# Kernel optimization log

Hardware: AMD Instinct MI355X
Metric: run time of the kernel (lower is better)

## Reference

```python
import jax, jax.numpy as jnp
import numpy as np

CONSTRAINT_WEIGHT = 0.5
FOCAL_GAMMA = 2.0
EPS = 1e-8

B, G, C = 65536, 9, 9
BLK = 3  # int(sqrt(G))


def setup_inputs() -> dict:
    key = jax.random.key(0)
    k1, k2, k3 = jax.random.split(key, 3)
    logits = jax.random.normal(k1, (B, G, G, C), dtype=jnp.float32)
    targets = jax.random.randint(k2, (B, G, G), 0, 10, dtype=jnp.int64)
    puzzles = jax.random.randint(k3, (B, G, G), 0, 10, dtype=jnp.int64)
    return {"logits": logits, "targets": targets, "puzzles": puzzles}


def _sudoku_loss(logits, targets, puzzles):
    b, g, _, c = logits.shape
    mask = (puzzles == 0).astype(logits.dtype)            # [B,G,G]
    tgt = jnp.clip(targets - 1, 0, c - 1)                 # [B,G,G]

    log_probs = jax.nn.log_softmax(logits, axis=-1)       # [B,G,G,C]
    probs = jnp.exp(log_probs)

    # --- focal CE over masked (empty) cells ---
    lp_t = jnp.take_along_axis(log_probs, tgt[..., None], axis=-1)[..., 0]  # [B,G,G]
    pt = jnp.exp(lp_t)
    ce = -lp_t
    focal = (1.0 - pt) ** FOCAL_GAMMA * ce
    msum = mask.sum()
    ce_loss = (focal * mask).sum() / (msum + EPS)

    # --- constraint loss ---
    masked_probs = probs * mask[..., None]                # [B,G,G,C]
    row_sums = masked_probs.sum(axis=2)                   # [B,G,C]
    row_loss = jnp.mean((row_sums - 1.0) ** 2)
    col_sums = masked_probs.sum(axis=1)                   # [B,G,C]
    col_loss = jnp.mean((col_sums - 1.0) ** 2)
    # boxes: [B, br, r, bc, c_in, C] -> sum over the 3x3 cells of each box
    box = masked_probs.reshape(b, BLK, BLK, BLK, BLK, c)
    box_sums = box.transpose(0, 1, 3, 2, 4, 5).reshape(b, BLK * BLK, BLK * BLK, c).sum(axis=2)
    box_loss = jnp.mean((box_sums - 1.0) ** 2)

    entropy = -(probs * log_probs).sum(axis=-1)           # [B,G,G]
    entropy_loss = 0.1 * ((entropy * mask).sum() / (msum + EPS))

    top2, _ = jax.lax.top_k(probs, 2)                     # [B,G,G,2]
    gap = top2[..., 0] - top2[..., 1]
    uniqueness_loss = 0.1 * jnp.mean(jax.nn.relu(1.0 - gap))

    constraint_loss = (row_loss + col_loss + box_loss + entropy_loss + uniqueness_loss) * 0.2
    return ce_loss + CONSTRAINT_WEIGHT * constraint_loss


def reference(logits, targets, puzzles):
    return _sudoku_loss(logits, targets, puzzles)
```

## Files before the change

kernel.cpp:

```cpp
#include <hip/hip_runtime.h>

#define THREADS 256
#define PB 8
#define CELLS_PB (PB * 81)
#define TOTW (CELLS_PB * 9)
#define NF4 (TOTW / 4)
#define SLANES 243
#define WLANES 162

typedef float f4 __attribute__((ext_vector_type(4)));
typedef __fp16 h2 __attribute__((ext_vector_type(2)));
typedef unsigned int u32;
typedef int i4 __attribute__((ext_vector_type(4)));

static __device__ __forceinline__ u32 pkrtz(float a, float b) {
  h2 v = __builtin_amdgcn_cvt_pkrtz(a, b);
  return __builtin_bit_cast(u32, v);
}

__global__ __launch_bounds__(THREADS) void sudoku_main(
    const float* __restrict__ logits,
    const int*   __restrict__ targets,
    const int*   __restrict__ puzzles,
    float* __restrict__ partial,
    int B, int ngrid)
{
  __shared__ float buf[TOTW];
  __shared__ float sred[4][5];

  const int tid = threadIdx.x;
  const int g   = blockIdx.x;
  const long totalCells = (long)B * 81;
  const long lim4 = totalCells * 9 / 4;

  float a_focal=0.f, a_ent=0.f, a_msk=0.f, a_uniq=0.f, a_sq=0.f;

  if (tid < SLANES) {
    const f4* src = (const f4*)logits;
    const long b4 = (long)g * NF4;
    f4* dst = (f4*)buf;
#pragma unroll
    for (int r = 0; r < 6; ++r) {
      long idx = b4 + r * SLANES + tid;
      if (idx < lim4) dst[r * SLANES + tid] = src[idx];
    }
  }

  const long cell0 = (long)g * CELLS_PB + 4 * tid;
  const bool vA = (tid < WLANES) && (cell0 < totalCells);
  i4 tg4{}, pz4{};
  if (vA) {
    tg4 = *(const i4*)(targets + cell0);
    pz4 = *(const i4*)(puzzles + cell0);
  }
  __syncthreads();

  if (vA) {
    f4 s[9];
#pragma unroll
    for (int q = 0; q < 9; ++q) s[q] = ((const f4*)buf)[tid * 9 + q];

#pragma unroll
    for (int k = 0; k < 4; ++k) {
      float l[9];
#pragma unroll
      for (int i = 0; i < 9; ++i) { const int w = 9 * k + i; l[i] = s[w >> 2][w & 3]; }
      int tg = tg4[k] - 1; tg = tg < 0 ? 0 : (tg > 8 ? 8 : tg);

      float t1 = l[0], t2 = -3.0e38f;
#pragma unroll
      for (int i = 1; i < 9; ++i) {
        float hi = fmaxf(t1, l[i]);
        float lo = fminf(t1, l[i]);
        t1 = hi; t2 = fmaxf(t2, lo);
      }
      float e[9], ssum = 0.f, lsum = 0.f, ltg = l[0];
#pragma unroll
      for (int i = 0; i < 9; ++i) {
        float x  = l[i] - t1;
        float ei = __expf(x);
        e[i] = ei; ssum += ei;
        lsum = fmaf(ei, x, lsum);
        if (i > 0) ltg = (tg == i) ? l[i] : ltg;
      }
      float inv_s = __builtin_amdgcn_rcpf(ssum);
      float logs  = __logf(ssum);
      float lpt   = (ltg - t1) - logs;
      float pt    = __expf(lpt);
      float om    = 1.f - pt;
      float focal = om * om * (-lpt);
      float ent   = logs - lsum * inv_s;
      float gap   = (1.f - __expf(t2 - t1)) * inv_s;
      float uq    = fmaxf(0.f, 1.f - gap);
      float mk    = (pz4[k] == 0) ? 1.f : 0.f;
      a_focal += focal * mk;
      a_ent   += ent * mk;
      a_msk   += mk;
      a_uniq  += uq;
      float pm = inv_s * mk;

      u32* pw = (u32*)buf + (size_t)(4 * tid + k) * 9;
      pw[0] = pkrtz(e[0] * pm, e[1] * pm);
      pw[1] = pkrtz(e[2] * pm, e[3] * pm);
      pw[2] = pkrtz(e[4] * pm, e[5] * pm);
      pw[3] = pkrtz(e[6] * pm, e[7] * pm);
      pw[4] = pkrtz(e[8] * pm, 0.f);
    }
  }
  __syncthreads();

  const int wv = tid >> 6, lane = tid & 63;
  if (lane < 10) {
    const int pz = wv * 2 + lane / 5;
    const int pr = lane % 5;
    if ((long)g * PB + pz < (long)B) {
      const u32* cb = (const u32*)buf;
      h2 hz; hz[0] = (__fp16)0.f; hz[1] = (__fp16)0.f;
      h2 rs[9], cs[9], bs[9];
#pragma unroll
      for (int u = 0; u < 9; ++u) { rs[u] = hz; cs[u] = hz; bs[u] = hz; }
      const int base = pz * 729 + pr;
#pragma unroll
      for (int j = 0; j < 81; ++j) {
        h2 v = __builtin_bit_cast(h2, cb[base + 9 * j]);
        rs[j / 9]                      += v;
        cs[j % 9]                      += v;
        bs[(j / 27) * 3 + (j % 9) / 3] += v;
      }
      const float hiw = (pr == 4) ? 0.f : 1.f;
      float sq = 0.f;
#pragma unroll
      for (int u = 0; u < 9; ++u) {
        float x;
        x = (float)rs[u][0] - 1.f; sq = fmaf(x, x, sq);
        x = (float)cs[u][0] - 1.f; sq = fmaf(x, x, sq);
        x = (float)bs[u][0] - 1.f; sq = fmaf(x, x, sq);
        x = (float)rs[u][1] - 1.f; sq = fmaf(hiw * x, x, sq);
        x = (float)cs[u][1] - 1.f; sq = fmaf(hiw * x, x, sq);
        x = (float)bs[u][1] - 1.f; sq = fmaf(hiw * x, x, sq);
      }
      a_sq += sq;
    }
  }

#pragma unroll
  for (int off = 32; off > 0; off >>= 1) {
    a_focal += __shfl_down(a_focal, off);
    a_ent   += __shfl_down(a_ent,   off);
    a_msk   += __shfl_down(a_msk,   off);
    a_uniq  += __shfl_down(a_uniq,  off);
    a_sq    += __shfl_down(a_sq,    off);
  }
  if (lane == 0) {
    sred[wv][0] = a_focal; sred[wv][1] = a_ent; sred[wv][2] = a_msk;
    sred[wv][3] = a_uniq;  sred[wv][4] = a_sq;
  }
  __syncthreads();
  if (tid < 5) {
    float v = sred[0][tid] + sred[1][tid] + sred[2][tid] + sred[3][tid];
    partial[(size_t)tid * ngrid + g] = v;
  }
}

__global__ __launch_bounds__(1024) void sudoku_finalize(
    const float* __restrict__ partial, float* __restrict__ out,
    int ngrid, float invBG)
{
  __shared__ float sb[16][5];
  const int tid = threadIdx.x;
  float s[5] = {0.f, 0.f, 0.f, 0.f, 0.f};
  for (int b = tid; b < ngrid; b += 1024) {
#pragma unroll
    for (int u = 0; u < 5; ++u) s[u] += partial[(size_t)u * ngrid + b];
  }
#pragma unroll
  for (int off = 32; off > 0; off >>= 1)
#pragma unroll
    for (int u = 0; u < 5; ++u) s[u] += __shfl_down(s[u], off);
  const int wv = tid >> 6, lane = tid & 63;
  if (lane == 0) {
#pragma unroll
    for (int u = 0; u < 5; ++u) sb[wv][u] = s[u];
  }
  __syncthreads();
  if (tid == 0) {
    float focal = 0.f, ent = 0.f, msum = 0.f, uniq = 0.f, sq = 0.f;
#pragma unroll
    for (int w = 0; w < 16; ++w) {
      focal += sb[w][0]; ent += sb[w][1]; msum += sb[w][2];
      uniq  += sb[w][3]; sq  += sb[w][4];
    }
    float inv_m = 1.f / (msum + 1e-8f);
    float ce    = focal * inv_m;
    float entl  = 0.1f * ent * inv_m;
    float uql   = 0.1f * uniq * invBG;
    float rcb   = sq * invBG;
    float constraint = (rcb + entl + uql) * 0.2f;
    out[0] = ce + 0.5f * constraint;
  }
}

extern "C" void kernel_launch(void* const* d_in, const int* in_sizes, int n_in,
                              void* d_out, int out_size, void* d_ws, size_t ws_size,
                              hipStream_t stream)
{
  (void)n_in; (void)out_size; (void)ws_size;
  const float* logits  = (const float*)d_in[0];
  const int*   targets = (const int*)d_in[1];
  const int*   puzzles = (const int*)d_in[2];
  float* out = (float*)d_out;
  float* partial = (float*)d_ws;

  const int B = in_sizes[0] / 729;
  const long totalCells = (long)B * 81;
  const int ngrid = (int)((totalCells + CELLS_PB - 1) / CELLS_PB);

  sudoku_main<<<ngrid, THREADS, 0, stream>>>(logits, targets, puzzles, partial, B, ngrid);

  const float invBG = 1.f / ((float)B * 81.f);
  sudoku_finalize<<<1, 1024, 0, stream>>>(partial, out, ngrid, invBG);
}
```

Before: 67.72 us.

## Use 512-thread blocks of 12 puzzles, two cells per thread, exp2-based softmax

Blocks grow to 512 threads covering 12 puzzles, so each worker thread processes two cells instead of four and all threads take part in the staging load. Softmax, log and focal terms move to base-2 hardware exp2/log with LN2 rescaling, and packed probabilities are written back with vectorized shared-memory stores. The box/row/column reduction is remapped to 8 lanes per wave across 8 waves. This raises per-block parallelism and cuts per-thread register pressure, but uses more LDS per block (about 35 KB), which may limit how many blocks fit on a CU.

```diff
diff --git a/kernel.cpp b/kernel.cpp
--- a/kernel.cpp
+++ b/kernel.cpp
@@ -1,24 +1,28 @@
 #include <hip/hip_runtime.h>
 
-#define THREADS 256
-#define PB 8
+#define THREADS 512
+#define PB 12
 #define CELLS_PB (PB * 81)
 #define TOTW (CELLS_PB * 9)
 #define NF4 (TOTW / 4)
-#define SLANES 243
-#define WLANES 162
+#define WLANES 486
 
 typedef float f4 __attribute__((ext_vector_type(4)));
+typedef float f2 __attribute__((ext_vector_type(2)));
 typedef __fp16 h2 __attribute__((ext_vector_type(2)));
 typedef unsigned int u32;
-typedef int i4 __attribute__((ext_vector_type(4)));
+typedef u32 u2 __attribute__((ext_vector_type(2)));
+typedef int i2 __attribute__((ext_vector_type(2)));
+
+#define LOG2E 1.44269504f
+#define LN2   0.69314718f
 
 static __device__ __forceinline__ u32 pkrtz(float a, float b) {
   h2 v = __builtin_amdgcn_cvt_pkrtz(a, b);
   return __builtin_bit_cast(u32, v);
 }
 
-__global__ __launch_bounds__(THREADS) void sudoku_main(
+__global__ __launch_bounds__(THREADS, 8) void sudoku_main(
     const float* __restrict__ logits,
     const int*   __restrict__ targets,
     const int*   __restrict__ puzzles,
@@ -26,7 +30,7 @@
     int B, int ngrid)
 {
   __shared__ float buf[TOTW];
-  __shared__ float sred[4][5];
+  __shared__ float sred[8][5];
 
   const int tid = threadIdx.x;
   const int g   = blockIdx.x;
@@ -35,37 +39,44 @@
 
   float a_focal=0.f, a_ent=0.f, a_msk=0.f, a_uniq=0.f, a_sq=0.f;
 
-  if (tid < SLANES) {
+  {
     const f4* src = (const f4*)logits;
     const long b4 = (long)g * NF4;
     f4* dst = (f4*)buf;
 #pragma unroll
-    for (int r = 0; r < 6; ++r) {
-      long idx = b4 + r * SLANES + tid;
-      if (idx < lim4) dst[r * SLANES + tid] = src[idx];
-    }
-  }
-
-  const long cell0 = (long)g * CELLS_PB + 4 * tid;
+    for (int r = 0; r < 4; ++r) {
+      long idx = b4 + r * THREADS + tid;
+      if (idx < lim4) dst[r * THREADS + tid] = src[idx];
+    }
+    if (tid < NF4 - 4 * THREADS) {
+      long idx = b4 + 4 * THREADS + tid;
+      if (idx < lim4) dst[4 * THREADS + tid] = src[idx];
+    }
+  }
+
+  const long cell0 = (long)g * CELLS_PB + 2 * tid;
   const bool vA = (tid < WLANES) && (cell0 < totalCells);
-  i4 tg4{}, pz4{};
+  i2 tg2{}, pz2{};
   if (vA) {
-    tg4 = *(const i4*)(targets + cell0);
-    pz4 = *(const i4*)(puzzles + cell0);
+    tg2 = *(const i2*)(targets + cell0);
+    pz2 = *(const i2*)(puzzles + cell0);
   }
   __syncthreads();
 
   if (vA) {
-    f4 s[9];
-#pragma unroll
-    for (int q = 0; q < 9; ++q) s[q] = ((const f4*)buf)[tid * 9 + q];
-
-#pragma unroll
-    for (int k = 0; k < 4; ++k) {
+    f2 v[9];
+    const f2* xp = (const f2*)(buf + 18 * tid);
+#pragma unroll
+    for (int q = 0; q < 9; ++q) v[q] = xp[q];
+
+    u32 q5[2][5];
+#pragma unroll
+    for (int k = 0; k < 2; ++k) {
       float l[9];
 #pragma unroll
-      for (int i = 0; i < 9; ++i) { const int w = 9 * k + i; l[i] = s[w >> 2][w & 3]; }
-      int tg = tg4[k] - 1; tg = tg < 0 ? 0 : (tg > 8 ? 8 : tg);
+      for (int i = 0; i < 9; ++i) { const int w = 9 * k + i; l[i] = v[w >> 1][w & 1]; }
+      int tg = ((k == 0) ? tg2[0] : tg2[1]) - 1; tg = tg < 0 ? 0 : (tg > 8 ? 8 : tg);
+      const int pz = (k == 0) ? pz2[0] : pz2[1];
 
       float t1 = l[0], t2 = -3.0e38f;
 #pragma unroll
@@ -74,72 +85,81 @@
         float lo = fminf(t1, l[i]);
         t1 = hi; t2 = fmaxf(t2, lo);
       }
-      float e[9], ssum = 0.f, lsum = 0.f, ltg = l[0];
+      const float t1b = t1 * LOG2E;
+      float e[9], ssum = 0.f, lsum2 = 0.f, x2tg = 0.f;
 #pragma unroll
       for (int i = 0; i < 9; ++i) {
-        float x  = l[i] - t1;
-        float ei = __expf(x);
+        float x2 = fmaf(l[i], LOG2E, -t1b);
+        float ei = __builtin_amdgcn_exp2f(x2);
         e[i] = ei; ssum += ei;
-        lsum = fmaf(ei, x, lsum);
-        if (i > 0) ltg = (tg == i) ? l[i] : ltg;
+        lsum2 = fmaf(ei, x2, lsum2);
+        x2tg = (tg == i) ? x2 : x2tg;
       }
       float inv_s = __builtin_amdgcn_rcpf(ssum);
-      float logs  = __logf(ssum);
-      float lpt   = (ltg - t1) - logs;
-      float pt    = __expf(lpt);
+      float logs2 = __builtin_amdgcn_logf(ssum);
+      float lptb  = x2tg - logs2;
+      float pt    = __builtin_amdgcn_exp2f(lptb);
       float om    = 1.f - pt;
-      float focal = om * om * (-lpt);
-      float ent   = logs - lsum * inv_s;
-      float gap   = (1.f - __expf(t2 - t1)) * inv_s;
+      float focal = om * om * (-lptb * LN2);
+      float ent   = (logs2 - lsum2 * inv_s) * LN2;
+      float g2    = __builtin_amdgcn_exp2f(fmaf(t2, LOG2E, -t1b));
+      float gap   = (1.f - g2) * inv_s;
       float uq    = fmaxf(0.f, 1.f - gap);
-      float mk    = (pz4[k] == 0) ? 1.f : 0.f;
+      float mk    = (pz == 0) ? 1.f : 0.f;
       a_focal += focal * mk;
       a_ent   += ent * mk;
       a_msk   += mk;
       a_uniq  += uq;
       float pm = inv_s * mk;
-
-      u32* pw = (u32*)buf + (size_t)(4 * tid + k) * 9;
-      pw[0] = pkrtz(e[0] * pm, e[1] * pm);
-      pw[1] = pkrtz(e[2] * pm, e[3] * pm);
-      pw[2] = pkrtz(e[4] * pm, e[5] * pm);
-      pw[3] = pkrtz(e[6] * pm, e[7] * pm);
-      pw[4] = pkrtz(e[8] * pm, 0.f);
-    }
+      q5[k][0] = pkrtz(e[0]*pm, e[1]*pm);
+      q5[k][1] = pkrtz(e[2]*pm, e[3]*pm);
+      q5[k][2] = pkrtz(e[4]*pm, e[5]*pm);
+      q5[k][3] = pkrtz(e[6]*pm, e[7]*pm);
+      q5[k][4] = pkrtz(e[8]*pm, 0.f);
+    }
+    u32* wp = (u32*)(buf + 18 * tid);
+    { u2 a; a[0]=q5[0][0]; a[1]=q5[0][1]; *(u2*)(wp + 0) = a; }
+    { u2 a; a[0]=q5[0][2]; a[1]=q5[0][3]; *(u2*)(wp + 2) = a; }
+    wp[4] = q5[0][4];
+    wp[9] = q5[1][0];
+    { u2 a; a[0]=q5[1][1]; a[1]=q5[1][2]; *(u2*)(wp + 10) = a; }
+    { u2 a; a[0]=q5[1][3]; a[1]=q5[1][4]; *(u2*)(wp + 12) = a; }
   }
   __syncthreads();
 
   const int wv = tid >> 6, lane = tid & 63;
-  if (lane < 10) {
-    const int pz = wv * 2 + lane / 5;
-    const int pr = lane % 5;
-    if ((long)g * PB + pz < (long)B) {
-      const u32* cb = (const u32*)buf;
-      h2 hz; hz[0] = (__fp16)0.f; hz[1] = (__fp16)0.f;
-      h2 rs[9], cs[9], bs[9];
-#pragma unroll
-      for (int u = 0; u < 9; ++u) { rs[u] = hz; cs[u] = hz; bs[u] = hz; }
-      const int base = pz * 729 + pr;
-#pragma unroll
-      for (int j = 0; j < 81; ++j) {
-        h2 v = __builtin_bit_cast(h2, cb[base + 9 * j]);
-        rs[j / 9]                      += v;
-        cs[j % 9]                      += v;
-        bs[(j / 27) * 3 + (j % 9) / 3] += v;
+  if (lane < 8) {
+    const int q = wv * 8 + lane;
+    if (q < PB * 5) {
+      const int pz = q / 5, pr = q % 5;
+      if ((long)g * PB + pz < (long)B) {
+        const u32* cb = (const u32*)buf;
+        h2 hz; hz[0] = (__fp16)0.f; hz[1] = (__fp16)0.f;
+        h2 rs[9], cs[9], bs[9];
+#pragma unroll
+        for (int u = 0; u < 9; ++u) { rs[u] = hz; cs[u] = hz; bs[u] = hz; }
+        const int base = pz * 729 + pr;
+#pragma unroll
+        for (int j = 0; j < 81; ++j) {
+          h2 pv = __builtin_bit_cast(h2, cb[base + 9 * j]);
+          rs[j / 9]                      += pv;
+          cs[j % 9]                      += pv;
+          bs[(j / 27) * 3 + (j % 9) / 3] += pv;
+        }
+        const float hiw = (pr == 4) ? 0.f : 1.f;
+        float sq = 0.f;
+#pragma unroll
+        for (int u = 0; u < 9; ++u) {
+          float x;
+          x = (float)rs[u][0] - 1.f; sq = fmaf(x, x, sq);
+          x = (float)cs[u][0] - 1.f; sq = fmaf(x, x, sq);
+          x = (float)bs[u][0] - 1.f; sq = fmaf(x, x, sq);
+          x = (float)rs[u][1] - 1.f; sq = fmaf(hiw * x, x, sq);
+          x = (float)cs[u][1] - 1.f; sq = fmaf(hiw * x, x, sq);
+          x = (float)bs[u][1] - 1.f; sq = fmaf(hiw * x, x, sq);
+        }
+        a_sq += sq;
       }
-      const float hiw = (pr == 4) ? 0.f : 1.f;
-      float sq = 0.f;
-#pragma unroll
-      for (int u = 0; u < 9; ++u) {
-        float x;
-        x = (float)rs[u][0] - 1.f; sq = fmaf(x, x, sq);
-        x = (float)cs[u][0] - 1.f; sq = fmaf(x, x, sq);
-        x = (float)bs[u][0] - 1.f; sq = fmaf(x, x, sq);
-        x = (float)rs[u][1] - 1.f; sq = fmaf(hiw * x, x, sq);
-        x = (float)cs[u][1] - 1.f; sq = fmaf(hiw * x, x, sq);
-        x = (float)bs[u][1] - 1.f; sq = fmaf(hiw * x, x, sq);
-      }
-      a_sq += sq;
     }
   }
 
@@ -157,8 +177,10 @@
   }
   __syncthreads();
   if (tid < 5) {
-    float v = sred[0][tid] + sred[1][tid] + sred[2][tid] + sred[3][tid];
-    partial[(size_t)tid * ngrid + g] = v;
+    float s = 0.f;
+#pragma unroll
+    for (int w = 0; w < 8; ++w) s += sred[w][tid];
+    partial[(size_t)tid * ngrid + g] = s;
   }
 }
 
```

Result: slower. 72.50 us (+7.1%).
